# Kernel optimization log

Measured on AMD Instinct MI355X. Metric: run time of the kernel, lower is better.

Reference implementation:

```python
import jax, jax.numpy as jnp
import numpy as np

N, E, G = 50000, 500000, 32
H, D = 4, 40  # heads, per-head dim; hidden = H*D = 160
HID, JK = H * D, 2 * H * D  # 160, 320


def setup_inputs() -> dict:
    key = jax.random.key(0)
    ks = jax.random.split(key, 32)
    s = 0.05
    inp = {
        'x': jax.random.normal(ks[0], (N, 5), jnp.float32),
        'edge_index': jax.random.randint(ks[1], (2, E), 0, N, jnp.int32).astype(jnp.int64),
        'edge_attr': jax.random.normal(ks[2], (E, 4), jnp.float32),
        'batch': jnp.sort(jax.random.randint(ks[3], (N,), 0, G, jnp.int32)).astype(jnp.int64),
        'W_in': jax.random.normal(ks[4], (5, HID), jnp.float32) * s,
        'b_in': jnp.zeros((HID,), jnp.float32),
        'Wq': jax.random.normal(ks[5], (2, HID, HID), jnp.float32) * s,
        'bq': jnp.zeros((2, HID), jnp.float32),
        'Wk': jax.random.normal(ks[6], (2, HID, HID), jnp.float32) * s,
        'bk': jnp.zeros((2, HID), jnp.float32),
        'Wv': jax.random.normal(ks[7], (2, HID, HID), jnp.float32) * s,
        'bv': jnp.zeros((2, HID), jnp.float32),
        'We': jax.random.normal(ks[8], (2, 4, HID), jnp.float32) * s,
        'be': jnp.zeros((2, HID), jnp.float32),
        'Wskip': jax.random.normal(ks[9], (2, HID, HID), jnp.float32) * s,
        'bskip': jnp.zeros((2, HID), jnp.float32),
        'Wbeta': jax.random.normal(ks[10], (2, 3 * HID, 1), jnp.float32) * s,
        'Wg1': jax.random.normal(ks[11], (JK, JK // 2), jnp.float32) * s,
        'bg1': jnp.zeros((JK // 2,), jnp.float32),
        'Wg2': jax.random.normal(ks[12], (JK // 2, 1), jnp.float32) * s,
        'bg2': jnp.zeros((1,), jnp.float32),
        'Wh1': jax.random.normal(ks[13], (JK, JK), jnp.float32) * s,
        'bh1': jnp.zeros((JK,), jnp.float32),
        'Wh2': jax.random.normal(ks[14], (JK, 6), jnp.float32) * s,
        'bh2': jnp.zeros((6,), jnp.float32),
    }
    return inp


def _transformer_conv(h, src, dst, edge_attr, Wq, bq, Wk, bk, Wv, bv, We, be, Wskip, bskip, Wbeta):
    n = h.shape[0]
    q = (h @ Wq + bq).reshape(n, H, D)
    k = (h @ Wk + bk).reshape(n, H, D)
    v = (h @ Wv + bv).reshape(n, H, D)
    e = (edge_attr @ We + be).reshape(-1, H, D)   # [E,H,D]
    k_e = k[src] + e                              # key with edge feature
    v_e = v[src] + e                              # value with edge feature
    alpha = jnp.einsum('ehd,ehd->eh', q[dst], k_e) / jnp.sqrt(jnp.float32(D))  # [E,H]
    # segment softmax over incoming edges of each destination node
    amax = jax.ops.segment_max(alpha, dst, num_segments=n)
    ex = jnp.exp(alpha - amax[dst])
    denom = jax.ops.segment_sum(ex, dst, num_segments=n)
    a = ex / denom[dst]                           # [E,H]
    out = jax.ops.segment_sum(v_e * a[..., None], dst, num_segments=n).reshape(n, H * D)
    # beta gate with skip connection
    r = h @ Wskip + bskip
    beta = jax.nn.sigmoid(jnp.concatenate([out, r, out - r], axis=-1) @ Wbeta)  # [n,1]
    return beta * r + (1.0 - beta) * out


def reference(x, edge_index, edge_attr, batch, W_in, b_in, Wq, bq, Wk, bk, Wv, bv,
              We, be, Wskip, bskip, Wbeta, Wg1, bg1, Wg2, bg2, Wh1, bh1, Wh2, bh2):
    src, dst = edge_index[0], edge_index[1]
    h = x @ W_in + b_in
    xs = []
    for l in range(2):
        h = _transformer_conv(h, src, dst, edge_attr, Wq[l], bq[l], Wk[l], bk[l],
                              Wv[l], bv[l], We[l], be[l], Wskip[l], bskip[l], Wbeta[l])
        xs.append(h)
    xc = jnp.concatenate(xs, axis=-1)             # JumpingKnowledge 'cat' -> [N,320]
    # AttentionalAggregation: gate MLP + segment softmax over graphs
    gate = jax.nn.relu(xc @ Wg1 + bg1) @ Wg2 + bg2  # [N,1]
    gmax = jax.ops.segment_max(gate, batch, num_segments=G)
    ge = jnp.exp(gate - gmax[batch])
    gden = jax.ops.segment_sum(ge, batch, num_segments=G)
    att = ge / gden[batch]
    pooled = jax.ops.segment_sum(att * xc, batch, num_segments=G)  # [G,320]
    out = jax.nn.relu(pooled @ Wh1 + bh1) @ Wh2 + bh2              # [G,6]
    return out.reshape(-1, 2, 3)
```

## Files before the change

### kernel.cpp

```cpp
#include <hip/hip_runtime.h>
#include <math.h>
#include <stddef.h>

#define NHEAD 4
#define DHEAD 40
#define HIDW 160
#define JKW 320
#define NGRAPH 32
#define BCAP 64

typedef __attribute__((ext_vector_type(8))) short short8;
typedef __attribute__((ext_vector_type(4))) float f32x4;
typedef __attribute__((ext_vector_type(2))) float f32x2;
typedef __fp16 h2 __attribute__((ext_vector_type(2)));
typedef int i32x4 __attribute__((ext_vector_type(4)));
typedef i32x4 i32x4_a4 __attribute__((aligned(4)));

__device__ inline unsigned short f2bf(float x){
  unsigned u = __float_as_uint(x);
  u += 0x7fff + ((u >> 16) & 1);
  return (unsigned short)(u >> 16);
}
__device__ inline float bf2f(unsigned short h){
  return __uint_as_float(((unsigned)h) << 16);
}
__device__ inline float fdot2(h2 a, h2 b, float c){
  return __builtin_amdgcn_fdot2(a, b, c, false);
}
__device__ inline h2 pk(float a, float b){
  return __builtin_amdgcn_cvt_pkrtz(a, b);
}
union HU { h2 h; int i; unsigned u; float f; };
__device__ inline h2 shfl_h2(h2 v, int xm){
  HU u; u.h = v; u.i = __shfl_xor(u.i, xm); return u.h;
}
__device__ inline h2 asH2(unsigned i){ HU u; u.u = i; return u.h; }

#if __has_builtin(__builtin_amdgcn_cvt_pk_f16_fp8)
__device__ inline h2 cvt8(int s){ return __builtin_amdgcn_cvt_pk_f16_fp8((short)s); }
#else
__device__ inline h2 cvt8(int s){
  f32x2 t = __builtin_amdgcn_cvt_pk_f32_fp8(s, false);
  return pk(t.x, t.y);
}
#endif

__device__ inline int lbound(const int* __restrict__ b, int N, int g){
  int lo = 0, hi = N;
  while (lo < hi){ int mid = (lo + hi) >> 1; if (b[mid] < g) lo = mid + 1; else hi = mid; }
  return lo;
}

__global__ __launch_bounds__(256) void k_pre(const float* __restrict__ x, const float* __restrict__ W_in,
                                             const float* __restrict__ b_in, unsigned short* __restrict__ hb,
                                             const float* __restrict__ Wq, const float* __restrict__ Wk,
                                             const float* __restrict__ Wv, const float* __restrict__ Ws,
                                             const float* __restrict__ bq, const float* __restrict__ bk,
                                             const float* __restrict__ bv, const float* __restrict__ bs,
                                             const float* __restrict__ Wg1,
                                             unsigned short* __restrict__ Bth, float* __restrict__ bp,
                                             unsigned short* __restrict__ Btgh,
                                             int* __restrict__ cnt, float* __restrict__ gate,
                                             float* __restrict__ pooled, int N){
  int NL = (N*20 + 255)/256;
  int bid = blockIdx.x, tid = threadIdx.x;
  if (bid < NL){
    int idx = bid*256 + tid;
    if (idx >= N*20) return;
    int n = idx / 20, j8 = (idx % 20)*8;
    const float* xr = x + n*5;
    float x0 = xr[0], x1 = xr[1], x2 = xr[2], x3 = xr[3], x4 = xr[4];
    float v[8];
    #pragma unroll
    for (int u = 0; u < 8; ++u) v[u] = b_in[j8+u];
    #pragma unroll
    for (int c = 0; c < 5; ++c){
      float xc = (c==0)?x0:(c==1)?x1:(c==2)?x2:(c==3)?x3:x4;
      const float4 wa = *(const float4*)(W_in + c*HIDW + j8);
      const float4 wb = *(const float4*)(W_in + c*HIDW + j8 + 4);
      v[0] += xc*wa.x; v[1] += xc*wa.y; v[2] += xc*wa.z; v[3] += xc*wa.w;
      v[4] += xc*wb.x; v[5] += xc*wb.y; v[6] += xc*wb.z; v[7] += xc*wb.w;
    }
    short8 o;
    #pragma unroll
    for (int u = 0; u < 8; ++u) o[u] = (short)f2bf(v[u]);
    *(short8*)(hb + (size_t)n*JKW + j8) = o;
  } else if (bid < NL + 1005){
    int idx = (bid - NL)*256 + tid;
    if (idx < 204800){
      int l = idx / 102400, r = idx % 102400;
      int i = r / 640, j = r % 640;
      int sel = j / HIDW, jj = j % HIDW;
      const float* W = (sel==0) ? Wq : (sel==1) ? Wk : (sel==2) ? Wv : Ws;
      Bth[(size_t)l*102400 + (size_t)j*160 + i] = f2bf(W[(size_t)l*25600 + i*HIDW + jj]);
    } else if (idx < 256000){
      int r = idx - 204800;
      int j = r / 320, i = r % 320;
      Btgh[(size_t)j*320 + i] = f2bf(Wg1[(size_t)i*160 + j]);
    } else if (idx < 257280){
      int r = idx - 256000;
      int l = r / 640, j = r % 640;
      int sel = j / HIDW, jj = j % HIDW;
      const float* bb = (sel==0) ? bq : (sel==1) ? bk : (sel==2) ? bv : bs;
      bp[l*640 + j] = bb[l*160 + jj];
    }
  } else {
    int idx = (bid - NL - 1005)*256 + tid;
    if (idx < N){ cnt[idx] = 0; gate[idx] = 0.f; }
    if (idx < NGRAPH*JKW) pooled[idx] = 0.f;
  }
}

__global__ __launch_bounds__(256) void k_fill(const int* __restrict__ dst, const int* __restrict__ src,
                                              const float* __restrict__ edge_attr, int E,
                                              int* __restrict__ cnt, uint4* __restrict__ edges){
  int e = blockIdx.x*256 + threadIdx.x;
  if (e < E){
    int d = dst[e];
    int p = atomicAdd(&cnt[d], 1);
    if (p < BCAP){
      float4 ea = *(const float4*)(edge_attr + (size_t)e*4);
      HU a, b; a.h = pk(ea.x, ea.y); b.h = pk(ea.z, ea.w);
      edges[(size_t)d*BCAP + p] = make_uint4((unsigned)src[e], a.u, b.u, 0u);
    }
  }
}

#define BSTR 40
#define BSTR1 164
template<int NSUB, int MODE>
__global__ __launch_bounds__(256) void k_mgemm(const unsigned short* __restrict__ A, int lda,
                                               const unsigned short* __restrict__ Bh,
                                               const float* __restrict__ bias,
                                               _Float16* __restrict__ qh,
                                               unsigned char* __restrict__ kv8,
                                               _Float16* __restrict__ rskip,
                                               const float* __restrict__ Wg2,
                                               float* __restrict__ gate,
                                               int M, int K){
  __shared__ short sBh[(MODE==1) ? (16*NSUB*BSTR1) : (2*16*NSUB*BSTR)];
  int tid = threadIdx.x;
  int wv = tid >> 6, lane = tid & 63;
  int quad = lane >> 4, l16 = lane & 15;

  int P = gridDim.x, MBy = gridDim.y;
  int bid = blockIdx.y * P + blockIdx.x;
  int fullRows = (MBy >> 3) << 3;
  int rowB, panel;
  if (bid < fullRows * P){
    int group = bid / (8*P), rem = bid % (8*P);
    rowB  = group*8 + (rem & 7);
    panel = rem >> 3;
  } else {
    int rem = bid - fullRows*P;
    int R = MBy - fullRows;
    panel = rem / R;
    rowB  = fullRows + rem % R;
  }
  int m0 = rowB*128 + wv*32;
  int col0 = panel * (16*NSUB);

  int ar0 = m0 + l16;      if (ar0 >= M) ar0 = M - 1;
  int ar1 = m0 + 16 + l16; if (ar1 >= M) ar1 = M - 1;
  const unsigned short* Ap0 = A + (size_t)ar0*lda + quad*8;
  const unsigned short* Ap1 = A + (size_t)ar1*lda + quad*8;

  f32x4 acc[2][NSUB];
  #pragma unroll
  for (int g = 0; g < 2; ++g)
    #pragma unroll
    for (int s = 0; s < NSUB; ++s) acc[g][s] = (f32x4){0.f,0.f,0.f,0.f};

  if constexpr (MODE == 1){
    for (int u = tid; u < 16*NSUB*20; u += 256){
      int col = u / 20, q = u % 20;
      *(short8*)(&sBh[col*BSTR1 + q*8]) =
        *(const short8*)(Bh + (size_t)(col0 + col)*K + q*8);
    }
    __syncthreads();
    #pragma unroll
    for (int kk = 0; kk < 5; ++kk){
      int k0 = kk << 5;
      short8 ah0 = *(const short8*)(Ap0 + k0);
      short8 ah1 = *(const short8*)(Ap1 + k0);
      #pragma unroll
      for (int s = 0; s < NSUB; ++s){
        short8 bh = *(const short8*)(&sBh[(s*16 + l16)*BSTR1 + k0 + quad*8]);
        acc[0][s] = __builtin_amdgcn_mfma_f32_16x16x32_bf16(ah0, bh, acc[0][s], 0, 0, 0);
        acc[1][s] = __builtin_amdgcn_mfma_f32_16x16x32_bf16(ah1, bh, acc[1][s], 0, 0, 0);
      }
    }
  } else {
    const int CH = K >> 5;
    for (int u = tid; u < 16*NSUB*4; u += 256){
      int col = u >> 2, q4 = u & 3;
      *(short8*)(&sBh[col*BSTR + q4*8]) =
        *(const short8*)(Bh + (size_t)(col0 + col)*K + q4*8);
    }
    __syncthreads();
    int buf = 0;
    for (int kk = 0; kk < CH; ++kk){
      int k0 = kk << 5;
      if (kk + 1 < CH){
        int kn = k0 + 32;
        for (int u = tid; u < 16*NSUB*4; u += 256){
          int col = u >> 2, q4 = u & 3;
          *(short8*)(&sBh[(buf^1)*16*NSUB*BSTR + col*BSTR + q4*8]) =
            *(const short8*)(Bh + (size_t)(col0 + col)*K + kn + q4*8);
        }
      }
      short8 ah0 = *(const short8*)(Ap0 + k0);
      short8 ah1 = *(const short8*)(Ap1 + k0);
      #pragma unroll
      for (int s = 0; s < NSUB; ++s){
        short8 bh = *(const short8*)(&sBh[buf*16*NSUB*BSTR + (s*16 + l16)*BSTR + quad*8]);
        acc[0][s] = __builtin_amdgcn_mfma_f32_16x16x32_bf16(ah0, bh, acc[0][s], 0, 0, 0);
        acc[1][s] = __builtin_amdgcn_mfma_f32_16x16x32_bf16(ah1, bh, acc[1][s], 0, 0, 0);
      }
      __syncthreads();
      buf ^= 1;
    }
  }

  const float qscale = 0.15811388300841898f;
  if (MODE == 1){
    #pragma unroll
    for (int g = 0; g < 2; ++g){
      #pragma unroll
      for (int s = 0; s < NSUB; ++s){
        int col = col0 + s*16 + l16;
        float bv = bias[col];
        int sel = col / 160, cc = col % 160;
        #pragma unroll
        for (int r = 0; r < 4; ++r){
          int row = m0 + g*16 + quad*4 + r;
          if (row >= M) continue;
          float v = acc[g][s][r] + bv;
          if (sel == 0)      qh[(size_t)row*160 + cc] = (_Float16)(v * qscale);
          else if (sel == 3) rskip[(size_t)row*160 + cc] = (_Float16)v;
          else {
            int slot = (cc/40)*4 + (cc%40)/10, j = cc%10;
            int e8 = __builtin_amdgcn_cvt_pk_fp8_f32(v, v, 0, false);
            kv8[(size_t)row*320 + slot*20 + (sel==2?10:0) + j] = (unsigned char)(e8 & 0xff);
          }
        }
      }
    }
  } else {
    float pg[2][4];
    #pragma unroll
    for (int g = 0; g < 2; ++g)
      #pragma unroll
      for (int r = 0; r < 4; ++r) pg[g][r] = 0.f;
    #pragma unroll
    for (int s = 0; s < NSUB; ++s){
      int col = col0 + s*16 + l16;
      float bv = bias[col], wg = Wg2[col];
      #pragma unroll
      for (int g = 0; g < 2; ++g)
        #pragma unroll
        for (int r = 0; r < 4; ++r)
          pg[g][r] += fmaxf(acc[g][s][r] + bv, 0.f) * wg;
    }
    #pragma unroll
    for (int g = 0; g < 2; ++g)
      #pragma unroll
      for (int r = 0; r < 4; ++r){
        float v = pg[g][r];
        v += __shfl_xor(v, 1); v += __shfl_xor(v, 2);
        v += __shfl_xor(v, 4); v += __shfl_xor(v, 8);
        int row = m0 + g*16 + quad*4 + r;
        if (l16 == 0 && row < M) atomicAdd(&gate[row], v);
      }
  }
}

__global__ __launch_bounds__(256) void k_qprep(const _Float16* __restrict__ qh,
                                               const float* __restrict__ We, const float* __restrict__ be,
                                               float* __restrict__ qwb, int N){
  int idx = blockIdx.x*256 + threadIdx.x;
  if (idx >= N*4) return;
  int n = idx >> 2, h = idx & 3;
  const unsigned* qp = (const unsigned*)(qh + (size_t)n*160 + h*40);
  float w0=0.f,w1=0.f,w2=0.f,w3=0.f,b=0.f;
  #pragma unroll
  for (int i = 0; i < 20; ++i){
    HU u; u.u = qp[i];
    float qa = (float)u.h.x, qb = (float)u.h.y;
    int c = h*40 + 2*i;
    w0 += qa*We[c]       + qb*We[c+1];
    w1 += qa*We[160+c]   + qb*We[161+c];
    w2 += qa*We[320+c]   + qb*We[321+c];
    w3 += qa*We[480+c]   + qb*We[481+c];
    b  += qa*be[c]       + qb*be[c+1];
  }
  float* o = qwb + (size_t)idx*5;
  o[0]=w0; o[1]=w1; o[2]=w2; o[3]=w3; o[4]=b;
}

__global__ __launch_bounds__(256) void k_attn(const _Float16* __restrict__ qh,
                                              const unsigned char* __restrict__ kv8,
                                              const _Float16* __restrict__ rskip,
                                              const float* __restrict__ qwb,
                                              const uint4* __restrict__ edges,
                                              const int* __restrict__ cnt,
                                              const float* __restrict__ We, const float* __restrict__ be,
                                              const float* __restrict__ Wb,
                                              unsigned short* __restrict__ hb,
                                              int loff, int N){
  int n = blockIdx.x*4 + (threadIdx.x >> 6);
  if (n >= N) return;
  int lane = threadIdx.x & 63;
  int g4 = lane >> 4;
  int w  = lane & 15;
  int hh = w & 3, t = w >> 2;
  int cbase = DHEAD*hh + 10*t;
  int slot = hh*4 + t;

  h2 qh2[5];
  {
    const unsigned* qp = (const unsigned*)(qh + (size_t)n*160 + cbase);
    #pragma unroll
    for (int i = 0; i < 5; ++i){ HU u; u.u = qp[i]; qh2[i] = u.h; }
  }
  const float* qwp = qwb + ((size_t)n*4 + hh)*5;
  float qw0 = qwp[0], qw1 = qwp[1], qw2 = qwp[2], qw3 = qwp[3], qb = qwp[4];
  h2 qw01 = pk(qw0, qw1), qw23 = pk(qw2, qw3);

  float ssum = 0.f;
  h2 zh = pk(0.f, 0.f);
  h2 acch[5], sah[2];
  #pragma unroll
  for (int i = 0; i < 5; ++i) acch[i] = zh;
  sah[0] = zh; sah[1] = zh;

  int deg = cnt[n]; if (deg > BCAP) deg = BCAP;
  int st = n*BCAP, en = st + deg;
  int B = (deg + 3) >> 2;

  int snA=0, snB=0, snC=0; bool vA=false, vB=false, vC=false;
  h2 eaA0=zh, eaA1=zh, eaB0=zh, eaB1=zh, eaC0=zh, eaC1=zh;
  {
    int p0 = st + g4;       vA = (p0 < en);
    if (vA){ uint4 e = edges[p0]; snA = (int)e.x; eaA0 = asH2(e.y); eaA1 = asH2(e.z); }
    int p1 = st + 4 + g4;   vB = (p1 < en);
    if (vB){ uint4 e = edges[p1]; snB = (int)e.x; eaB0 = asH2(e.y); eaB1 = asH2(e.z); }
    int p2 = st + 8 + g4;   vC = (p2 < en);
    if (vC){ uint4 e = edges[p2]; snC = (int)e.x; eaC0 = asH2(e.y); eaC1 = asH2(e.z); }
  }
  i32x4 cA0 = {0,0,0,0}, cB0 = {0,0,0,0}; int cA4 = 0, cB4 = 0;
  if (vA){
    const unsigned char* kp = kv8 + (size_t)snA*320 + slot*20;
    cA0 = *(const i32x4_a4*)kp; cA4 = *(const int*)(kp+16);
  }
  if (vB){
    const unsigned char* kp = kv8 + (size_t)snB*320 + slot*20;
    cB0 = *(const i32x4_a4*)kp; cB4 = *(const int*)(kp+16);
  }

  for (int b = 0; b < B; ++b){
    int snD = 0; h2 eaD0 = zh, eaD1 = zh; bool vD;
    int p3 = st + (b+3)*4 + g4;
    vD = (p3 < en);
    if (vD){ uint4 e = edges[p3]; snD = (int)e.x; eaD0 = asH2(e.y); eaD1 = asH2(e.z); }
    i32x4 cC0 = {0,0,0,0}; int cC4 = 0;
    if (vC){
      const unsigned char* kp = kv8 + (size_t)snC*320 + slot*20;
      cC0 = *(const i32x4_a4*)kp; cC4 = *(const int*)(kp+16);
    }
    float p = 0.f;
    if (vA){
      p = fdot2(qh2[0], cvt8(cA0.x), p);
      p = fdot2(qh2[1], cvt8(cA0.x >> 16), p);
      p = fdot2(qh2[2], cvt8(cA0.y), p);
      p = fdot2(qh2[3], cvt8(cA0.y >> 16), p);
      p = fdot2(qh2[4], cvt8(cA0.z), p);
    }
    p += __shfl_xor(p, 4);
    p += __shfl_xor(p, 8);
    p += qb;
    p = fdot2(eaA0, qw01, p);
    p = fdot2(eaA1, qw23, p);

    if (vA){
      float ex = __expf(p);
      ssum += ex;
      h2 eh = pk(ex, ex);
      acch[0] += cvt8(cA0.z >> 16)*eh;
      acch[1] += cvt8(cA0.w)*eh;
      acch[2] += cvt8(cA0.w >> 16)*eh;
      acch[3] += cvt8(cA4)*eh;
      acch[4] += cvt8(cA4 >> 16)*eh;
      sah[0] += eaA0*eh;
      sah[1] += eaA1*eh;
    }
    snA = snB; vA = vB; eaA0 = eaB0; eaA1 = eaB1; cA0 = cB0; cA4 = cB4;
    snB = snC; vB = vC; eaB0 = eaC0; eaB1 = eaC1; cB0 = cC0; cB4 = cC4;
    snC = snD; vC = vD; eaC0 = eaD0; eaC1 = eaD1;
  }

  #pragma unroll
  for (int xm = 16; xm < 64; xm <<= 1){
    ssum += __shfl_xor(ssum, xm);
    #pragma unroll
    for (int i = 0; i < 5; ++i) acch[i] += shfl_h2(acch[i], xm);
    sah[0] += shfl_h2(sah[0], xm);
    sah[1] += shfl_h2(sah[1], xm);
  }

  {
    float inv = (ssum > 0.f) ? 1.f/ssum : 0.f;
    float sw0 = (float)sah[0].x*inv, sw1 = (float)sah[0].y*inv;
    float sw2 = (float)sah[1].x*inv, sw3 = (float)sah[1].y*inv;
    float bterm = (ssum > 0.f) ? 1.f : 0.f;

    float a0 = (g4==0) ? (float)acch[0].x : (g4==1) ? (float)acch[0].y
             : (g4==2) ? (float)acch[1].x : (float)acch[1].y;
    float a1 = (g4==0) ? (float)acch[2].x : (g4==1) ? (float)acch[2].y
             : (g4==2) ? (float)acch[3].x : (float)acch[3].y;
    float a2 = (g4==0) ? (float)acch[4].x : (float)acch[4].y;

    const _Float16* rp = rskip + (size_t)n*160 + cbase;
    float ov[3], rrv[3];
    float part = 0.f;
    #pragma unroll
    for (int jj = 0; jj < 3; ++jj){
      int j = g4 + 4*jj;
      float aj = (jj==0) ? a0 : (jj==1) ? a1 : a2;
      ov[jj] = 0.f; rrv[jj] = 0.f;
      if (j < 10){
        int c = cbase + j;
        float o = aj*inv + sw0*We[c] + sw1*We[160+c] + sw2*We[320+c] + sw3*We[480+c] + bterm*be[c];
        float r = (float)rp[j];
        ov[jj] = o; rrv[jj] = r;
        part += o*Wb[c] + r*Wb[160+c] + (o-r)*Wb[320+c];
      }
    }
    #pragma unroll
    for (int xm = 1; xm < 64; xm <<= 1) part += __shfl_xor(part, xm);
    float beta = 1.f/(1.f + __expf(-part));
    unsigned short* hp = hb + (size_t)n*JKW + loff + cbase;
    #pragma unroll
    for (int jj = 0; jj < 3; ++jj){
      int j = g4 + 4*jj;
      if (j < 10) hp[j] = f2bf(beta*rrv[jj] + (1.f-beta)*ov[jj]);
    }
  }
}

__global__ __launch_bounds__(320) void k_pool(const unsigned short* __restrict__ hb, const float* __restrict__ gate,
                                              const int* __restrict__ batch, int N,
                                              float* __restrict__ pooled){
  __shared__ float sm[320];
  int g = blockIdx.x, part = blockIdx.y, j = threadIdx.x;
  int lo = lbound(batch, N, g), hi = lbound(batch, N, g+1);
  int len = hi - lo;
  if (len <= 0) return;
  float m = -INFINITY;
  for (int i = lo + j; i < hi; i += 320) m = fmaxf(m, gate[i]);
  sm[j] = m; __syncthreads();
  #pragma unroll
  for (int off = 256; off; off >>= 1){
    if (j < off && j + off < 320) sm[j] = fmaxf(sm[j], sm[j+off]);
    __syncthreads();
  }
  float gm = sm[0]; __syncthreads();
  float s = 0.f;
  for (int i = lo + j; i < hi; i += 320) s += __expf(gate[i] - gm);
  sm[j] = s; __syncthreads();
  #pragma unroll
  for (int off = 256; off; off >>= 1){
    if (j < off && j + off < 320) sm[j] += sm[j+off];
    __syncthreads();
  }
  float dg = sm[0];
  float invd = (dg > 0.f) ? 1.f/dg : 0.f;

  int chunk = (len + (int)gridDim.y - 1) / (int)gridDim.y;
  int a = lo + part*chunk;
  int bnd = a + chunk; if (bnd > hi) bnd = hi;
  if (a >= bnd) return;
  float acc = 0.f;
  for (int n = a; n < bnd; ++n){
    float at = __expf(gate[n] - gm);
    acc += at * bf2f(hb[(size_t)n*JKW + j]);
  }
  atomicAdd(&pooled[g*JKW + j], acc*invd);
}

__global__ __launch_bounds__(320) void k_head(const float* __restrict__ pooled, const float* __restrict__ Wh1,
                                              const float* __restrict__ bh1, const float* __restrict__ Wh2,
                                              const float* __restrict__ bh2, float* __restrict__ out){
  __shared__ float p[320];
  __shared__ float t[320];
  int g = blockIdx.x, tid = threadIdx.x;
  p[tid] = pooled[g*JKW + tid]; __syncthreads();
  float a = bh1[tid];
  for (int i = 0; i < 320; ++i) a += p[i]*Wh1[i*JKW + tid];
  t[tid] = fmaxf(a, 0.f); __syncthreads();
  if (tid < 6){
    float o = bh2[tid];
    for (int j = 0; j < 320; ++j) o += t[j]*Wh2[j*6 + tid];
    out[g*6 + tid] = o;
  }
}

extern "C" void kernel_launch(void* const* d_in, const int* in_sizes, int n_in,
                              void* d_out, int out_size, void* d_ws, size_t ws_size,
                              hipStream_t stream){
  (void)n_in; (void)out_size; (void)ws_size;
  const float* x        = (const float*)d_in[0];
  const int*   eidx     = (const int*)d_in[1];
  const float* edge_attr= (const float*)d_in[2];
  const int*   batch    = (const int*)d_in[3];
  const float* W_in     = (const float*)d_in[4];
  const float* b_in     = (const float*)d_in[5];
  const float* Wq       = (const float*)d_in[6];
  const float* bq       = (const float*)d_in[7];
  const float* Wk       = (const float*)d_in[8];
  const float* bk       = (const float*)d_in[9];
  const float* Wv       = (const float*)d_in[10];
  const float* bv       = (const float*)d_in[11];
  const float* We       = (const float*)d_in[12];
  const float* be       = (const float*)d_in[13];
  const float* Wsk      = (const float*)d_in[14];
  const float* bsk      = (const float*)d_in[15];
  const float* Wb       = (const float*)d_in[16];
  const float* Wg1      = (const float*)d_in[17];
  const float* bg1      = (const float*)d_in[18];
  const float* Wg2      = (const float*)d_in[19];
  const float* Wh1      = (const float*)d_in[21];
  const float* bh1      = (const float*)d_in[22];
  const float* Wh2      = (const float*)d_in[23];
  const float* bh2      = (const float*)d_in[24];

  const int N = in_sizes[0] / 5;
  const int E = in_sizes[1] / 2;
  float* out = (float*)d_out;

  char* w = (char*)d_ws;
  auto alloc = [&](size_t bytes)->char*{ char* p = w; w += (bytes + 255) & ~(size_t)255; return p; };
  unsigned short* hb = (unsigned short*)alloc((size_t)N*JKW*2);
  _Float16* qh  = (_Float16*)alloc((size_t)N*160*2);
  unsigned char* kv8 = (unsigned char*)alloc((size_t)N*320);
  _Float16* rskip = (_Float16*)alloc((size_t)N*160*2);
  float* qwb    = (float*)alloc((size_t)N*20*4);
  unsigned short* Bth  = (unsigned short*)alloc((size_t)2*640*160*2);
  unsigned short* Btgh = (unsigned short*)alloc((size_t)160*320*2);
  float* bpack  = (float*)alloc((size_t)2*640*4);
  int*   cnt    = (int*)alloc((size_t)N*4);
  uint4* edges  = (uint4*)alloc((size_t)N*BCAP*16);
  float* gate   = (float*)alloc((size_t)N*4);
  float* pooled = (float*)alloc(NGRAPH*JKW*4);

  const int* srcI = eidx;
  const int* dstI = eidx + E;

  const int NL = (N*20 + 255)/256;
  const int NZ = (N + 255)/256;
  k_pre<<<NL + 1005 + NZ, 256, 0, stream>>>(x, W_in, b_in, hb,
                                            Wq, Wk, Wv, Wsk, bq, bk, bv, bsk, Wg1,
                                            Bth, bpack, Btgh, cnt, gate, pooled, N);

  const int eb = (E + 255)/256;
  k_fill<<<eb, 256, 0, stream>>>(dstI, srcI, edge_attr, E, cnt, edges);

  const int MB128 = (N + 127)/128;
  for (int l = 0; l < 2; ++l){
    dim3 g1(5, MB128);
    k_mgemm<8,1><<<g1, 256, 0, stream>>>(hb, JKW, Bth + (size_t)l*102400, bpack + l*640,
                                         qh, kv8, rskip, nullptr, nullptr, N, HIDW);
    k_qprep<<<(N*4 + 255)/256, 256, 0, stream>>>(qh, We + l*640, be + l*160, qwb, N);
    k_attn<<<(N + 3)/4, 256, 0, stream>>>(qh, kv8, rskip, qwb, edges, cnt,
                                          We + l*640, be + l*160, Wb + l*480, hb, l*HIDW, N);
  }

  k_mgemm<10,2><<<dim3(1, MB128), 256, 0, stream>>>(hb, JKW, Btgh, bg1, nullptr, nullptr, nullptr,
                                                    Wg2, gate, N, JKW);

  dim3 g3(NGRAPH, 8);
  k_pool<<<g3, 320, 0, stream>>>(hb, gate, batch, N, pooled);
  k_head<<<NGRAPH, 320, 0, stream>>>(pooled, Wh1, bh1, Wh2, bh2, out);
}
```

Baseline: 481.2 us.

## Assign one 16-lane group per node in attention kernel instead of one wavefront

The attention kernel moves from one 64-lane wavefront per destination node, with four edge groups splitting the edges, to one 16-lane group per node that walks every edge serially. Four nodes now share a wavefront. This removes the cross-group shuffle reduction and the idle lanes that low-degree nodes leave, and lets the epilogue write packed 32-bit outputs. In exchange, each node's edge loop is four times longer and loop trip counts diverge within a wavefront because its four nodes have different degrees, which may expose more gather latency.

Result: faster. 456.8 us (-5.1%).

```diff
diff --git a/kernel.cpp b/kernel.cpp
--- a/kernel.cpp
+++ b/kernel.cpp
@@ -308,22 +308,23 @@
                                               const float* __restrict__ Wb,
                                               unsigned short* __restrict__ hb,
                                               int loff, int N){
-  int n = blockIdx.x*4 + (threadIdx.x >> 6);
-  if (n >= N) return;
-  int lane = threadIdx.x & 63;
-  int g4 = lane >> 4;
-  int w  = lane & 15;
+  int tid = threadIdx.x;
+  int grp = tid >> 4;
+  int n = blockIdx.x*16 + grp;
+  bool valid = (n < N);
+  int nn = valid ? n : (N-1);
+  int w = tid & 15;
   int hh = w & 3, t = w >> 2;
   int cbase = DHEAD*hh + 10*t;
   int slot = hh*4 + t;
 
   h2 qh2[5];
   {
-    const unsigned* qp = (const unsigned*)(qh + (size_t)n*160 + cbase);
-    #pragma unroll
-    for (int i = 0; i < 5; ++i){ HU u; u.u = qp[i]; qh2[i] = u.h; }
-  }
-  const float* qwp = qwb + ((size_t)n*4 + hh)*5;
+    const unsigned* qp = (const unsigned*)(qh + (size_t)nn*160 + cbase);
+    #pragma unroll
+    for (int i = 0; i < 5; ++i) qh2[i] = asH2(qp[i]);
+  }
+  const float* qwp = qwb + ((size_t)nn*4 + hh)*5;
   float qw0 = qwp[0], qw1 = qwp[1], qw2 = qwp[2], qw3 = qwp[3], qb = qwp[4];
   h2 qw01 = pk(qw0, qw1), qw23 = pk(qw2, qw3);
 
@@ -334,78 +335,52 @@
   for (int i = 0; i < 5; ++i) acch[i] = zh;
   sah[0] = zh; sah[1] = zh;
 
-  int deg = cnt[n]; if (deg > BCAP) deg = BCAP;
-  int st = n*BCAP, en = st + deg;
-  int B = (deg + 3) >> 2;
-
-  int snA=0, snB=0, snC=0; bool vA=false, vB=false, vC=false;
-  h2 eaA0=zh, eaA1=zh, eaB0=zh, eaB1=zh, eaC0=zh, eaC1=zh;
-  {
-    int p0 = st + g4;       vA = (p0 < en);
-    if (vA){ uint4 e = edges[p0]; snA = (int)e.x; eaA0 = asH2(e.y); eaA1 = asH2(e.z); }
-    int p1 = st + 4 + g4;   vB = (p1 < en);
-    if (vB){ uint4 e = edges[p1]; snB = (int)e.x; eaB0 = asH2(e.y); eaB1 = asH2(e.z); }
-    int p2 = st + 8 + g4;   vC = (p2 < en);
-    if (vC){ uint4 e = edges[p2]; snC = (int)e.x; eaC0 = asH2(e.y); eaC1 = asH2(e.z); }
-  }
-  i32x4 cA0 = {0,0,0,0}, cB0 = {0,0,0,0}; int cA4 = 0, cB4 = 0;
-  if (vA){
-    const unsigned char* kp = kv8 + (size_t)snA*320 + slot*20;
+  int deg = 0;
+  if (valid){ deg = cnt[nn]; if (deg > BCAP) deg = BCAP; }
+  int st = nn*BCAP;
+
+  uint4 recA = make_uint4(0,0,0,0), recB = make_uint4(0,0,0,0);
+  i32x4 cA0 = {0,0,0,0}; int cA4 = 0;
+  if (deg > 0) recA = edges[st];
+  if (deg > 1) recB = edges[st+1];
+  if (deg > 0){
+    const unsigned char* kp = kv8 + (size_t)recA.x*320 + slot*20;
     cA0 = *(const i32x4_a4*)kp; cA4 = *(const int*)(kp+16);
   }
-  if (vB){
-    const unsigned char* kp = kv8 + (size_t)snB*320 + slot*20;
-    cB0 = *(const i32x4_a4*)kp; cB4 = *(const int*)(kp+16);
-  }
-
-  for (int b = 0; b < B; ++b){
-    int snD = 0; h2 eaD0 = zh, eaD1 = zh; bool vD;
-    int p3 = st + (b+3)*4 + g4;
-    vD = (p3 < en);
-    if (vD){ uint4 e = edges[p3]; snD = (int)e.x; eaD0 = asH2(e.y); eaD1 = asH2(e.z); }
-    i32x4 cC0 = {0,0,0,0}; int cC4 = 0;
-    if (vC){
-      const unsigned char* kp = kv8 + (size_t)snC*320 + slot*20;
-      cC0 = *(const i32x4_a4*)kp; cC4 = *(const int*)(kp+16);
-    }
+
+  for (int e = 0; e < deg; ++e){
+    uint4 recC = make_uint4(0,0,0,0);
+    if (e + 2 < deg) recC = edges[st + e + 2];
+    i32x4 cB0 = {0,0,0,0}; int cB4 = 0;
+    if (e + 1 < deg){
+      const unsigned char* kp = kv8 + (size_t)recB.x*320 + slot*20;
+      cB0 = *(const i32x4_a4*)kp; cB4 = *(const int*)(kp+16);
+    }
+    h2 ea0 = asH2(recA.y), ea1 = asH2(recA.z);
     float p = 0.f;
-    if (vA){
-      p = fdot2(qh2[0], cvt8(cA0.x), p);
-      p = fdot2(qh2[1], cvt8(cA0.x >> 16), p);
-      p = fdot2(qh2[2], cvt8(cA0.y), p);
-      p = fdot2(qh2[3], cvt8(cA0.y >> 16), p);
-      p = fdot2(qh2[4], cvt8(cA0.z), p);
-    }
+    p = fdot2(qh2[0], cvt8(cA0.x), p);
+    p = fdot2(qh2[1], cvt8(cA0.x >> 16), p);
+    p = fdot2(qh2[2], cvt8(cA0.y), p);
+    p = fdot2(qh2[3], cvt8(cA0.y >> 16), p);
+    p = fdot2(qh2[4], cvt8(cA0.z), p);
     p += __shfl_xor(p, 4);
     p += __shfl_xor(p, 8);
     p += qb;
-    p = fdot2(eaA0, qw01, p);
-    p = fdot2(eaA1, qw23, p);
-
-    if (vA){
-      float ex = __expf(p);
-      ssum += ex;
-      h2 eh = pk(ex, ex);
-      acch[0] += cvt8(cA0.z >> 16)*eh;
-      acch[1] += cvt8(cA0.w)*eh;
-      acch[2] += cvt8(cA0.w >> 16)*eh;
-      acch[3] += cvt8(cA4)*eh;
-      acch[4] += cvt8(cA4 >> 16)*eh;
-      sah[0] += eaA0*eh;
-      sah[1] += eaA1*eh;
-    }
-    snA = snB; vA = vB; eaA0 = eaB0; eaA1 = eaB1; cA0 = cB0; cA4 = cB4;
-    snB = snC; vB = vC; eaB0 = eaC0; eaB1 = eaC1; cB0 = cC0; cB4 = cC4;
-    snC = snD; vC = vD; eaC0 = eaD0; eaC1 = eaD1;
-  }
-
-  #pragma unroll
-  for (int xm = 16; xm < 64; xm <<= 1){
-    ssum += __shfl_xor(ssum, xm);
-    #pragma unroll
-    for (int i = 0; i < 5; ++i) acch[i] += shfl_h2(acch[i], xm);
-    sah[0] += shfl_h2(sah[0], xm);
-    sah[1] += shfl_h2(sah[1], xm);
+    p = fdot2(ea0, qw01, p);
+    p = fdot2(ea1, qw23, p);
+
+    float ex = __expf(p);
+    ssum += ex;
+    h2 eh = pk(ex, ex);
+    acch[0] += cvt8(cA0.z >> 16)*eh;
+    acch[1] += cvt8(cA0.w)*eh;
+    acch[2] += cvt8(cA0.w >> 16)*eh;
+    acch[3] += cvt8(cA4)*eh;
+    acch[4] += cvt8(cA4 >> 16)*eh;
+    sah[0] += ea0*eh;
+    sah[1] += ea1*eh;
+
+    recA = recB; recB = recC; cA0 = cB0; cA4 = cB4;
   }
 
   {
@@ -414,36 +389,33 @@
     float sw2 = (float)sah[1].x*inv, sw3 = (float)sah[1].y*inv;
     float bterm = (ssum > 0.f) ? 1.f : 0.f;
 
-    float a0 = (g4==0) ? (float)acch[0].x : (g4==1) ? (float)acch[0].y
-             : (g4==2) ? (float)acch[1].x : (float)acch[1].y;
-    float a1 = (g4==0) ? (float)acch[2].x : (g4==1) ? (float)acch[2].y
-             : (g4==2) ? (float)acch[3].x : (float)acch[3].y;
-    float a2 = (g4==0) ? (float)acch[4].x : (float)acch[4].y;
-
-    const _Float16* rp = rskip + (size_t)n*160 + cbase;
-    float ov[3], rrv[3];
+    const unsigned* rpu = (const unsigned*)(rskip + (size_t)nn*160 + cbase);
+    float o[10];
     float part = 0.f;
     #pragma unroll
-    for (int jj = 0; jj < 3; ++jj){
-      int j = g4 + 4*jj;
-      float aj = (jj==0) ? a0 : (jj==1) ? a1 : a2;
-      ov[jj] = 0.f; rrv[jj] = 0.f;
-      if (j < 10){
-        int c = cbase + j;
-        float o = aj*inv + sw0*We[c] + sw1*We[160+c] + sw2*We[320+c] + sw3*We[480+c] + bterm*be[c];
-        float r = (float)rp[j];
-        ov[jj] = o; rrv[jj] = r;
-        part += o*Wb[c] + r*Wb[160+c] + (o-r)*Wb[320+c];
+    for (int i = 0; i < 5; ++i){
+      int c = cbase + 2*i;
+      float o0 = (float)acch[i].x*inv + sw0*We[c]   + sw1*We[160+c] + sw2*We[320+c] + sw3*We[480+c] + bterm*be[c];
+      float o1 = (float)acch[i].y*inv + sw0*We[c+1] + sw1*We[161+c] + sw2*We[321+c] + sw3*We[481+c] + bterm*be[c+1];
+      HU u; u.u = rpu[i];
+      float r0 = (float)u.h.x, r1 = (float)u.h.y;
+      part += o0*Wb[c]   + r0*Wb[160+c] + (o0-r0)*Wb[320+c];
+      part += o1*Wb[c+1] + r1*Wb[161+c] + (o1-r1)*Wb[321+c];
+      o[2*i] = o0; o[2*i+1] = o1;
+    }
+    part += __shfl_xor(part, 1); part += __shfl_xor(part, 2);
+    part += __shfl_xor(part, 4); part += __shfl_xor(part, 8);
+    float beta = 1.f/(1.f + __expf(-part));
+    if (valid){
+      unsigned* hp32 = (unsigned*)(hb + (size_t)nn*JKW + loff);
+      #pragma unroll
+      for (int i = 0; i < 5; ++i){
+        HU u; u.u = rpu[i];
+        float r0 = (float)u.h.x, r1 = (float)u.h.y;
+        unsigned lo = f2bf(beta*r0 + (1.f-beta)*o[2*i]);
+        unsigned hi = f2bf(beta*r1 + (1.f-beta)*o[2*i+1]);
+        hp32[cbase/2 + i] = lo | (hi << 16);
       }
-    }
-    #pragma unroll
-    for (int xm = 1; xm < 64; xm <<= 1) part += __shfl_xor(part, xm);
-    float beta = 1.f/(1.f + __expf(-part));
-    unsigned short* hp = hb + (size_t)n*JKW + loff + cbase;
-    #pragma unroll
-    for (int jj = 0; jj < 3; ++jj){
-      int j = g4 + 4*jj;
-      if (j < 10) hp[j] = f2bf(beta*rrv[jj] + (1.f-beta)*ov[jj]);
     }
   }
 }
@@ -571,8 +543,8 @@
     k_mgemm<8,1><<<g1, 256, 0, stream>>>(hb, JKW, Bth + (size_t)l*102400, bpack + l*640,
                                          qh, kv8, rskip, nullptr, nullptr, N, HIDW);
     k_qprep<<<(N*4 + 255)/256, 256, 0, stream>>>(qh, We + l*640, be + l*160, qwb, N);
-    k_attn<<<(N + 3)/4, 256, 0, stream>>>(qh, kv8, rskip, qwb, edges, cnt,
-                                          We + l*640, be + l*160, Wb + l*480, hb, l*HIDW, N);
+    k_attn<<<(N + 15)/16, 256, 0, stream>>>(qh, kv8, rskip, qwb, edges, cnt,
+                                            We + l*640, be + l*160, Wb + l*480, hb, l*HIDW, N);
   }
 
   k_mgemm<10,2><<<dim3(1, MB128), 256, 0, stream>>>(hb, JKW, Btgh, bg1, nullptr, nullptr, nullptr,
```
